# Performance work log

Hardware: AMD Instinct MI355X
Metric: run time of the kernel (lower is better)

The kernel has to match this reference:

```python
import jax, jax.numpy as jnp
import numpy as np

CLASSES = 21
IOU_THRESH = 0.5
ALPHA = 0.25   # focal loss alpha
GAMMA = 2.0    # focal loss gamma
SL1_BETA = 1.0 # torch SmoothL1Loss default beta
CLS_W = 1.0
REG_W = 1.0
NUM_ANCHORS = 98304
NUM_TARGETS = 1024


def _compute_iou(boxes_a, boxes_b):
    # boxes_a: [T,4], boxes_b: [A,4] in (x1,y1,x2,y2) -> [T,A]
    lt = jnp.maximum(boxes_a[:, None, :2], boxes_b[None, :, :2])
    rb = jnp.minimum(boxes_a[:, None, 2:], boxes_b[None, :, 2:])
    wh = jnp.clip(rb - lt, 0.0)
    inter = wh[..., 0] * wh[..., 1]
    area_a = (boxes_a[:, 2] - boxes_a[:, 0]) * (boxes_a[:, 3] - boxes_a[:, 1])
    area_b = (boxes_b[:, 2] - boxes_b[:, 0]) * (boxes_b[:, 3] - boxes_b[:, 1])
    union = area_a[:, None] + area_b[None, :] - inter
    return inter / jnp.maximum(union, 1e-8)


def _encode(boxes, anchors):
    bw = boxes[:, 2] - boxes[:, 0]
    bh = boxes[:, 3] - boxes[:, 1]
    bcx = boxes[:, 0] + 0.5 * bw
    bcy = boxes[:, 1] + 0.5 * bh
    aw = anchors[:, 2] - anchors[:, 0]
    ah = anchors[:, 3] - anchors[:, 1]
    acx = anchors[:, 0] + 0.5 * aw
    acy = anchors[:, 1] + 0.5 * ah
    tx = (bcx - acx) / aw
    ty = (bcy - acy) / ah
    tw = jnp.log(jnp.maximum(bw, 1e-8) / aw)
    th = jnp.log(jnp.maximum(bh, 1e-8) / ah)
    return jnp.stack([tx, ty, tw, th], axis=1)


def _focal_loss(logits, targets):
    # elementwise sigmoid focal loss (no reduction)
    p = jax.nn.sigmoid(logits)
    # numerically stable BCE with logits
    ce = jnp.maximum(logits, 0.0) - logits * targets + jnp.log1p(jnp.exp(-jnp.abs(logits)))
    p_t = p * targets + (1.0 - p) * (1.0 - targets)
    alpha_t = ALPHA * targets + (1.0 - ALPHA) * (1.0 - targets)
    return alpha_t * (1.0 - p_t) ** GAMMA * ce


def _smooth_l1(diff):
    ad = jnp.abs(diff)
    return jnp.where(ad < SL1_BETA, 0.5 * diff * diff / SL1_BETA, ad - 0.5 * SL1_BETA)


def setup_inputs() -> dict:
    key = jax.random.key(0)
    kA, kW, kT, kJ, kL, kC, kB = jax.random.split(key, 7)
    A, T = NUM_ANCHORS, NUM_TARGETS
    centers = jax.random.uniform(kA, (A, 2), minval=0.15, maxval=0.85)
    sizes = jax.random.uniform(kW, (A, 2), minval=0.05, maxval=0.30)
    anchors = jnp.concatenate([centers - 0.5 * sizes, centers + 0.5 * sizes], axis=1)
    # targets = jittered anchors so IoU >= 0.5 matches exist
    idx = jax.random.randint(kT, (T,), 0, A)
    jitter = jax.random.uniform(kJ, (T, 4), minval=-0.01, maxval=0.01)
    target_boxes = anchors[idx] + jitter
    target_labels = jax.random.randint(kL, (T,), 0, CLASSES)
    classification_preds = jax.random.normal(kC, (A, CLASSES), dtype=jnp.float32)
    boxes_preds = jax.random.normal(kB, (A, 4), dtype=jnp.float32)
    return {
        'classification_preds': classification_preds,
        'boxes_preds': boxes_preds,
        'anchors': anchors,
        'target_boxes': target_boxes,
        'target_labels': target_labels,
    }


def reference(classification_preds, boxes_preds, anchors, target_boxes, target_labels):
    iou = _compute_iou(target_boxes, anchors)  # [T, A]

    # anchor-side matching -> classification targets
    max_iou_for_anchors = jnp.max(iou, axis=0)          # [A]
    target_ids_for_anchors = jnp.argmax(iou, axis=0)     # [A]
    positive_mask = max_iou_for_anchors >= IOU_THRESH    # [A] bool
    n_pos = jnp.sum(positive_mask.astype(jnp.float32))
    onehot = jax.nn.one_hot(target_labels[target_ids_for_anchors], CLASSES, dtype=jnp.float32)
    cls_targets = jnp.where(positive_mask[:, None], onehot, 0.0)
    cls_loss = jnp.sum(_focal_loss(classification_preds, cls_targets)) / n_pos

    max_iou_for_targets = jnp.max(iou, axis=1)          # [T]
    anchor_ids_for_targets = jnp.argmax(iou, axis=1)     # [T]
    t_mask = (max_iou_for_targets >= IOU_THRESH).astype(jnp.float32)  # [T]
    matched_anchors = anchors[anchor_ids_for_targets]    # [T,4]
    encoded = _encode(target_boxes, matched_anchors)     # [T,4]
    pred = boxes_preds[anchor_ids_for_targets]           # [T,4]
    diff = (pred - encoded) * t_mask[:, None]
    n_match = jnp.maximum(jnp.sum(t_mask), 1.0)
    reg_loss = jnp.sum(_smooth_l1(diff)) / (n_match * 4.0)  # mean over matched elements

    w_cls = cls_loss * CLS_W
    w_reg = reg_loss * REG_W
    return (w_cls + w_reg, w_cls, w_reg)
```

## Files before the change

kernel.cpp:

```cpp
#include <hip/hip_runtime.h>
#include <stdint.h>

#define NA 98304
#define NT 1024
#define NC 21
#define NBLK 1536
#define HI_MIN 0xBF000000u
#define C3S 0.33333f

typedef unsigned int u32;
typedef unsigned long long u64;


__device__ __forceinline__ float f0(float x) {
    const float ax = fabsf(x);
    const float u  = __expf(-ax);
    const float ce = fmaxf(x, 0.f) + __logf(1.f + u);
    const float p  = (x >= 0.f ? 1.f : u) / (1.f + u);
    return 0.75f * p * p * ce;
}
__device__ __forceinline__ float f1(float x) {
    const float ax = fabsf(x);
    const float u  = __expf(-ax);
    const float ce = fmaxf(x, 0.f) - x + __logf(1.f + u);
    const float p  = (x >= 0.f ? 1.f : u) / (1.f + u);
    const float q  = 1.f - p;
    return 0.25f * q * q * ce;
}
__device__ __forceinline__ u64 mk_key(float iou, u32 idx) {
    return ((u64)(__float_as_uint(iou) | 0x80000000u) << 32) |
           (u64)(0xFFFFFFFFu - idx);
}
__device__ __forceinline__ float smooth_l1(float d) {
    const float ad = fabsf(d);
    return (ad < 1.f) ? 0.5f * d * d : ad - 0.5f;
}
__device__ __forceinline__ u64 aload64(const u64* p) {
    return __hip_atomic_load(p, __ATOMIC_RELAXED, __HIP_MEMORY_SCOPE_AGENT);
}
__device__ __forceinline__ float aloadf(const float* p) {
    return __hip_atomic_load(p, __ATOMIC_RELAXED, __HIP_MEMORY_SCOPE_AGENT);
}
__device__ __forceinline__ int aloadi(const int* p) {
    return __hip_atomic_load(p, __ATOMIC_RELAXED, __HIP_MEMORY_SCOPE_AGENT);
}

#define SCREEN(j, m)                                                        \
    {                                                                       \
        const float w0 = fminf(az4[j], tb.z) + fminf(negax[j], tb.x);       \
        const float w  = fmaxf(w0, 0.f);                                    \
        const float h0 = fminf(aw4[j], tb.w) + fminf(negay[j], tb.y);       \
        m |= (fmaf(w, h0, -ar34[j]) >= sac) ? (1ull << i) : 0ull;           \
    }

#define WALK(j, mj, bk)                                                     \
    if (mj != 0ull) {                                                       \
        u64 m = mj;                                                         \
        const float arj = (az4[j] + negax[j]) * (aw4[j] + negay[j]);        \
        do {                                                                \
            const int i = __ffsll(m) - 1;                                   \
            m &= m - 1;                                                     \
            const int t = tb0 + 4 * i;                                      \
            const float4 tb = s_t[t];                                       \
            const float sa = (tb.z + tb.x) * (tb.w + tb.y);                 \
            const float w = fmaxf(fminf(az4[j], tb.z) + fminf(negax[j], tb.x), 0.f); \
            const float h = fmaxf(fminf(aw4[j], tb.w) + fminf(negay[j], tb.y), 0.f); \
            const float inter = w * h;                                      \
            const float uni   = (arj + sa) - inter;                         \
            const float iou   = inter / uni;                                \
            const u64 ak = mk_key(iou, (u32)t);                             \
            if (ak > bk) bk = ak;                                           \
            atomicMax(&s_tk[t], mk_key(iou, (u32)(abase + j)));             \
        } while (m != 0ull);                                                \
    }

#define FOLD(bk)                                                            \
    {                                                                       \
        u64 o_ = __shfl_xor(bk, 16);                                        \
        if (o_ > bk) bk = o_;                                               \
        o_ = __shfl_xor(bk, 32);                                            \
        if (o_ > bk) bk = o_;                                               \
    }

__global__ __launch_bounds__(256) void k_all(
    const float* __restrict__ preds,
    const float4* __restrict__ preds4,
    const int* __restrict__ tlabels,
    const float4* __restrict__ anchors,
    const float4* __restrict__ tboxes,
    const float4* __restrict__ bpreds,
    u64* __restrict__ tkeys,
    float* __restrict__ part,
    int* __restrict__ npos_part,
    int* __restrict__ done_g,
    int* __restrict__ done2,
    float* __restrict__ out)
{
    __shared__ float4 s_t[NT];
    __shared__ u64 s_tk[NT];
    __shared__ u64 s_bk[4][64];
    __shared__ float  s_f[4];
    __shared__ int    s_fin;
    __shared__ double s_d[4];
    __shared__ int    s_i[4];
    __shared__ float  s_s[4], s_m[4];

    const int tid  = threadIdx.x;
    const int b    = blockIdx.x;
    const int lane = tid & 63, wid = tid >> 6;

    float4 tbl[4];
    #pragma unroll
    for (int k = 0; k < 4; ++k) tbl[k] = tboxes[tid + 256 * k];

    float facc;
    {
        const int pb = b * 336;
        const float4 v0 = preds4[pb + tid];
        facc = (f0(v0.x) + f0(v0.y)) + (f0(v0.z) + f0(v0.w));
        if (tid < 80) {
            const float4 v1 = preds4[pb + 256 + tid];
            facc += (f0(v1.x) + f0(v1.y)) + (f0(v1.z) + f0(v1.w));
        }
    }

    #pragma unroll
    for (int k = 0; k < 4; ++k) {
        s_t[tid + 256 * k]  = make_float4(-tbl[k].x, -tbl[k].y, tbl[k].z, tbl[k].w);
        s_tk[tid + 256 * k] = 0ull;
    }

    const int qd    = lane & 15;
    const int sl    = lane >> 4;
    const int abase = b * 64 + 4 * qd;
    float negax[4], negay[4], az4[4], aw4[4], ar34[4];
    #pragma unroll
    for (int j = 0; j < 4; ++j) {
        const float4 A = anchors[abase + j];
        negax[j] = -A.x; negay[j] = -A.y;
        az4[j]   = A.z;  aw4[j]   = A.w;
        ar34[j]  = ((A.z - A.x) * (A.w - A.y)) * C3S;
    }
    __syncthreads();

    u64 m0 = 0ull, m1 = 0ull, m2 = 0ull, m3 = 0ull;
    const int tb0 = wid * 256 + sl;
    #pragma unroll 16
    for (int i = 0; i < 64; ++i) {
        const float4 tb = s_t[tb0 + 4 * i];
        const float sa  = (tb.z + tb.x) * (tb.w + tb.y);
        const float sac = sa * C3S;
        SCREEN(0, m0)
        SCREEN(1, m1)
        SCREEN(2, m2)
        SCREEN(3, m3)
    }

    u64 bk0 = 0ull, bk1 = 0ull, bk2 = 0ull, bk3 = 0ull;
    WALK(0, m0, bk0)
    WALK(1, m1, bk1)
    WALK(2, m2, bk2)
    WALK(3, m3, bk3)

    FOLD(bk0) FOLD(bk1) FOLD(bk2) FOLD(bk3)
    if (sl == 0) {
        s_bk[wid][4 * qd + 0] = bk0;
        s_bk[wid][4 * qd + 1] = bk1;
        s_bk[wid][4 * qd + 2] = bk2;
        s_bk[wid][4 * qd + 3] = bk3;
    }

    for (int o = 32; o > 0; o >>= 1) facc += __shfl_down(facc, o);
    if (lane == 0) s_f[wid] = facc;
    __syncthreads();

    #pragma unroll
    for (int k = 0; k < 4; ++k) {
        const int t = tid + 256 * k;
        const u64 v = s_tk[t];
        if (v != 0ull) atomicMax(&tkeys[t], v);
    }

    float corrv = 0.f;
    int   cnt   = 0;
    if (tid < 64) {
        u64 k0 = s_bk[0][tid];
        const u64 k1 = s_bk[1][tid];
        const u64 k2 = s_bk[2][tid];
        const u64 k3 = s_bk[3][tid];
        if (k1 > k0) k0 = k1;
        if (k2 > k0) k0 = k2;
        if (k3 > k0) k0 = k3;
        if ((u32)(k0 >> 32) >= HI_MIN) {
            cnt = 1;
            const int tI  = (int)(0xFFFFFFFFu - (u32)k0);
            const int lab = tlabels[tI];
            const float x = preds[(b * 64 + tid) * NC + lab];
            corrv = f1(x) - f0(x);
        }
        for (int o = 32; o > 0; o >>= 1) {
            corrv += __shfl_down(corrv, o);
            cnt   += __shfl_down(cnt, o);
        }
    }
    if (tid == 0) {
        __hip_atomic_store(&part[b], (s_f[0] + s_f[1] + s_f[2] + s_f[3]) + corrv,
                           __ATOMIC_RELAXED, __HIP_MEMORY_SCOPE_AGENT);
        __hip_atomic_store(&npos_part[b], cnt,
                           __ATOMIC_RELAXED, __HIP_MEMORY_SCOPE_AGENT);
    }
    __syncthreads();
    if (tid == 0) {
        __threadfence();
        int fin = 0;
        if (atomicAdd(&done_g[b & 63], 1) == 23) {
            __threadfence();
            fin = (atomicAdd(done2, 1) == 63);
        }
        s_fin = fin;
    }
    __syncthreads();
    if (!s_fin) return;
    __builtin_amdgcn_fence(__ATOMIC_ACQUIRE, "agent");

    double cl = 0.0;
    int    np = 0;
    #pragma unroll
    for (int j = 0; j < 6; ++j) {
        const int i = tid + 256 * j;
        cl += (double)aloadf(&part[i]);
        np += aloadi(&npos_part[i]);
    }
    float s = 0.f, m = 0.f;
    #pragma unroll
    for (int j = 0; j < 4; ++j) {
        const int t = tid + 256 * j;
        const u64 key = aload64(&tkeys[t]);
        if ((u32)(key >> 32) >= HI_MIN) {
            const u32 ga = 0xFFFFFFFFu - (u32)key;
            const float4 tb  = tboxes[t];
            const float4 abx = anchors[ga];
            const float4 pb  = bpreds[ga];
            const float bw = tb.z - tb.x, bh = tb.w - tb.y;
            const float bcx = tb.x + 0.5f * bw, bcy = tb.y + 0.5f * bh;
            const float aw = abx.z - abx.x, ah = abx.w - abx.y;
            const float acx = abx.x + 0.5f * aw, acy = abx.y + 0.5f * ah;
            const float tx = (bcx - acx) / aw;
            const float ty = (bcy - acy) / ah;
            const float tw = logf(fmaxf(bw, 1e-8f) / aw);
            const float th = logf(fmaxf(bh, 1e-8f) / ah);
            s += smooth_l1(pb.x - tx) + smooth_l1(pb.y - ty) +
                 smooth_l1(pb.z - tw) + smooth_l1(pb.w - th);
            m += 1.f;
        }
    }
    for (int o = 32; o > 0; o >>= 1) {
        cl += __shfl_down(cl, o);
        np += __shfl_down(np, o);
        s  += __shfl_down(s, o);
        m  += __shfl_down(m, o);
    }
    __syncthreads();
    if (lane == 0) { s_d[wid] = cl; s_i[wid] = np; s_s[wid] = s; s_m[wid] = m; }
    __syncthreads();
    if (tid == 0) {
        const double cls_sum = s_d[0] + s_d[1] + s_d[2] + s_d[3];
        const int    npos    = s_i[0] + s_i[1] + s_i[2] + s_i[3];
        const float  rs      = s_s[0] + s_s[1] + s_s[2] + s_s[3];
        const float  rm      = s_m[0] + s_m[1] + s_m[2] + s_m[3];
        const float cls = (float)(cls_sum / (double)npos);
        const float reg = rs / (fmaxf(rm, 1.f) * 4.f);
        out[0] = cls + reg;
        out[1] = cls;
        out[2] = reg;
    }
}

extern "C" void kernel_launch(void* const* d_in, const int* in_sizes, int n_in,
                              void* d_out, int out_size, void* d_ws, size_t ws_size,
                              hipStream_t stream) {
    const float*  preds   = (const float*)d_in[0];
    const float4* preds4  = (const float4*)d_in[0];
    const float4* bpreds  = (const float4*)d_in[1];
    const float4* anchors = (const float4*)d_in[2];
    const float4* tboxes  = (const float4*)d_in[3];
    const int*    tlabels = (const int*)d_in[4];

    char* ws = (char*)d_ws;
    int*  done2     = (int*)(ws + 0);
    int*  done_g    = (int*)(ws + 128);
    float* part     = (float*)(ws + 1024);
    int*  npos_part = (int*)(ws + 8192);
    u64*  tkeys     = (u64*)(ws + 16384);

    hipMemsetAsync(d_ws, 0, 1024, stream);

    k_all<<<dim3(NBLK), 256, 0, stream>>>(
        preds, preds4, tlabels, anchors, tboxes, bpreds,
        tkeys, part, npos_part, done_g, done2, (float*)d_out);
}
```

Before: 124.4 us.

## Transpose IoU matching loop: threads own targets, iterate over block anchors

Restructures the fused IoU matching so each thread holds four target boxes in registers and loops over the block's 64 anchors read from shared memory, instead of each thread holding four anchors and scanning targets from shared memory with a screen-then-walk bitmask pass. Per-target maxima are kept in registers and pushed with global atomicMax directly, while per-anchor maxima go through shared-memory atomicMax. This removes the 1024-entry target staging in shared memory, the bitmask walk and the cross-wave shuffles. In exchange it adds divergent branches inside the inner loop and shared atomics per candidate pair.

After: 127.5 us. 1.02x slower.

```diff
diff --git a/kernel.cpp b/kernel.cpp
--- a/kernel.cpp
+++ b/kernel.cpp
@@ -45,41 +45,22 @@
     return __hip_atomic_load(p, __ATOMIC_RELAXED, __HIP_MEMORY_SCOPE_AGENT);
 }
 
-#define SCREEN(j, m)                                                        \
+#define CHECK(k, tkk)                                                       \
     {                                                                       \
-        const float w0 = fminf(az4[j], tb.z) + fminf(negax[j], tb.x);       \
+        const float w0 = fminf(ac.z, tz[k]) + fminf(ac.x, ntx[k]);          \
         const float w  = fmaxf(w0, 0.f);                                    \
-        const float h0 = fminf(aw4[j], tb.w) + fminf(negay[j], tb.y);       \
-        m |= (fmaf(w, h0, -ar34[j]) >= sac) ? (1ull << i) : 0ull;           \
-    }
-
-#define WALK(j, mj, bk)                                                     \
-    if (mj != 0ull) {                                                       \
-        u64 m = mj;                                                         \
-        const float arj = (az4[j] + negax[j]) * (aw4[j] + negay[j]);        \
-        do {                                                                \
-            const int i = __ffsll(m) - 1;                                   \
-            m &= m - 1;                                                     \
-            const int t = tb0 + 4 * i;                                      \
-            const float4 tb = s_t[t];                                       \
-            const float sa = (tb.z + tb.x) * (tb.w + tb.y);                 \
-            const float w = fmaxf(fminf(az4[j], tb.z) + fminf(negax[j], tb.x), 0.f); \
-            const float h = fmaxf(fminf(aw4[j], tb.w) + fminf(negay[j], tb.y), 0.f); \
+        const float h0 = fminf(ac.w, tw4[k]) + fminf(ac.y, nty[k]);         \
+        if (fmaf(w, h0, narc) >= sac[k]) {                                  \
+            const float h     = fmaxf(h0, 0.f);                             \
             const float inter = w * h;                                      \
+            const float arj   = (ac.z + ac.x) * (ac.w + ac.y);              \
+            const float sa    = (tz[k] + ntx[k]) * (tw4[k] + nty[k]);       \
             const float uni   = (arj + sa) - inter;                         \
             const float iou   = inter / uni;                                \
-            const u64 ak = mk_key(iou, (u32)t);                             \
-            if (ak > bk) bk = ak;                                           \
-            atomicMax(&s_tk[t], mk_key(iou, (u32)(abase + j)));             \
-        } while (m != 0ull);                                                \
-    }
-
-#define FOLD(bk)                                                            \
-    {                                                                       \
-        u64 o_ = __shfl_xor(bk, 16);                                        \
-        if (o_ > bk) bk = o_;                                               \
-        o_ = __shfl_xor(bk, 32);                                            \
-        if (o_ > bk) bk = o_;                                               \
+            const u64 nk = mk_key(iou, (u32)(b * 64 + j));                  \
+            if (nk > tkk) tkk = nk;                                         \
+            atomicMax(&s_ak[j], mk_key(iou, (u32)(t0 + 64 * k)));           \
+        }                                                                   \
     }
 
 __global__ __launch_bounds__(256) void k_all(
@@ -96,9 +77,9 @@
     int* __restrict__ done2,
     float* __restrict__ out)
 {
-    __shared__ float4 s_t[NT];
-    __shared__ u64 s_tk[NT];
-    __shared__ u64 s_bk[4][64];
+    __shared__ float4 s_anc[64];
+    __shared__ float  s_narc[64];
+    __shared__ u64    s_ak[64];
     __shared__ float  s_f[4];
     __shared__ int    s_fin;
     __shared__ double s_d[4];
@@ -109,9 +90,22 @@
     const int b    = blockIdx.x;
     const int lane = tid & 63, wid = tid >> 6;
 
-    float4 tbl[4];
+    if (tid < 64) {
+        const float4 A = anchors[b * 64 + tid];
+        s_anc[tid]  = make_float4(-A.x, -A.y, A.z, A.w);
+        s_narc[tid] = -(((A.z - A.x) * (A.w - A.y)) * C3S);
+        s_ak[tid]   = 0ull;
+    }
+
+    const int t0 = wid * 256 + lane;
+    float tz[4], ntx[4], tw4[4], nty[4], sac[4];
     #pragma unroll
-    for (int k = 0; k < 4; ++k) tbl[k] = tboxes[tid + 256 * k];
+    for (int k = 0; k < 4; ++k) {
+        const float4 tb = tboxes[t0 + 64 * k];
+        tz[k]  = tb.z;  ntx[k] = -tb.x;
+        tw4[k] = tb.w;  nty[k] = -tb.y;
+        sac[k] = ((tb.z - tb.x) * (tb.w - tb.y)) * C3S;
+    }
 
     float facc;
     {
@@ -124,73 +118,33 @@
         }
     }
 
-    #pragma unroll
-    for (int k = 0; k < 4; ++k) {
-        s_t[tid + 256 * k]  = make_float4(-tbl[k].x, -tbl[k].y, tbl[k].z, tbl[k].w);
-        s_tk[tid + 256 * k] = 0ull;
-    }
-
-    const int qd    = lane & 15;
-    const int sl    = lane >> 4;
-    const int abase = b * 64 + 4 * qd;
-    float negax[4], negay[4], az4[4], aw4[4], ar34[4];
-    #pragma unroll
-    for (int j = 0; j < 4; ++j) {
-        const float4 A = anchors[abase + j];
-        negax[j] = -A.x; negay[j] = -A.y;
-        az4[j]   = A.z;  aw4[j]   = A.w;
-        ar34[j]  = ((A.z - A.x) * (A.w - A.y)) * C3S;
-    }
-    __syncthreads();
-
-    u64 m0 = 0ull, m1 = 0ull, m2 = 0ull, m3 = 0ull;
-    const int tb0 = wid * 256 + sl;
-    #pragma unroll 16
-    for (int i = 0; i < 64; ++i) {
-        const float4 tb = s_t[tb0 + 4 * i];
-        const float sa  = (tb.z + tb.x) * (tb.w + tb.y);
-        const float sac = sa * C3S;
-        SCREEN(0, m0)
-        SCREEN(1, m1)
-        SCREEN(2, m2)
-        SCREEN(3, m3)
-    }
-
-    u64 bk0 = 0ull, bk1 = 0ull, bk2 = 0ull, bk3 = 0ull;
-    WALK(0, m0, bk0)
-    WALK(1, m1, bk1)
-    WALK(2, m2, bk2)
-    WALK(3, m3, bk3)
-
-    FOLD(bk0) FOLD(bk1) FOLD(bk2) FOLD(bk3)
-    if (sl == 0) {
-        s_bk[wid][4 * qd + 0] = bk0;
-        s_bk[wid][4 * qd + 1] = bk1;
-        s_bk[wid][4 * qd + 2] = bk2;
-        s_bk[wid][4 * qd + 3] = bk3;
+    u64 tk0 = 0ull, tk1 = 0ull, tk2 = 0ull, tk3 = 0ull;
+    __syncthreads();
+
+    #pragma unroll 8
+    for (int j = 0; j < 64; ++j) {
+        const float4 ac  = s_anc[j];
+        const float narc = s_narc[j];
+        CHECK(0, tk0)
+        CHECK(1, tk1)
+        CHECK(2, tk2)
+        CHECK(3, tk3)
     }
 
     for (int o = 32; o > 0; o >>= 1) facc += __shfl_down(facc, o);
     if (lane == 0) s_f[wid] = facc;
-    __syncthreads();
-
-    #pragma unroll
-    for (int k = 0; k < 4; ++k) {
-        const int t = tid + 256 * k;
-        const u64 v = s_tk[t];
-        if (v != 0ull) atomicMax(&tkeys[t], v);
-    }
+
+    if (tk0 != 0ull) atomicMax(&tkeys[t0],       tk0);
+    if (tk1 != 0ull) atomicMax(&tkeys[t0 +  64], tk1);
+    if (tk2 != 0ull) atomicMax(&tkeys[t0 + 128], tk2);
+    if (tk3 != 0ull) atomicMax(&tkeys[t0 + 192], tk3);
+
+    __syncthreads();
 
     float corrv = 0.f;
     int   cnt   = 0;
     if (tid < 64) {
-        u64 k0 = s_bk[0][tid];
-        const u64 k1 = s_bk[1][tid];
-        const u64 k2 = s_bk[2][tid];
-        const u64 k3 = s_bk[3][tid];
-        if (k1 > k0) k0 = k1;
-        if (k2 > k0) k0 = k2;
-        if (k3 > k0) k0 = k3;
+        const u64 k0 = s_ak[tid];
         if ((u32)(k0 >> 32) >= HI_MIN) {
             cnt = 1;
             const int tI  = (int)(0xFFFFFFFFu - (u32)k0);
```
